# Optimization experiments

Measured on AMD Instinct MI355X. Metric: run time of the kernel, lower is better.

## Reference

```python
import jax, jax.numpy as jnp
import numpy as np

B, S, T, D, H, FF = 2, 512, 64, 256, 8, 1024
DK = D // H
EPS = 1e-5


def setup_inputs() -> dict:
    key = jax.random.key(0)
    ks = jax.random.split(key, 24)
    sc = 1.0 / np.sqrt(D)
    inp = {"x": jax.random.normal(ks[0], (B, S, T, D), jnp.float32)}
    names = ["tq", "tk", "tv", "to", "sq", "sk", "sv", "so"]
    for i, n in enumerate(names):
        inp[n + "_w"] = jax.random.normal(ks[1 + 2 * i], (D, D), jnp.float32) * sc
        inp[n + "_b"] = jax.random.normal(ks[2 + 2 * i], (D,), jnp.float32) * sc
    inp["fc1_w"] = jax.random.normal(ks[17], (D, FF), jnp.float32) * sc
    inp["fc1_b"] = jnp.zeros((FF,), jnp.float32)
    inp["fc2_w"] = jax.random.normal(ks[18], (FF, D), jnp.float32) * (1.0 / np.sqrt(FF))
    inp["fc2_b"] = jnp.zeros((D,), jnp.float32)
    inp["ln1_w"] = jnp.ones((D,), jnp.float32)
    inp["ln1_b"] = jnp.zeros((D,), jnp.float32)
    inp["ln2_w"] = jnp.ones((D,), jnp.float32)
    inp["ln2_b"] = jnp.zeros((D,), jnp.float32)
    return inp


def _heads(x, w, b):
    # (B,S,T,D) -> (B,H,S,T,DK)
    Bx, Sx, Tx, Dx = x.shape
    return (x @ w + b).reshape(Bx, Sx, Tx, H, Dx // H).transpose(0, 3, 1, 2, 4)


def _merge(o, w, b):
    # (B,H,S,T,DK) -> (B,S,T,D)
    Bx, Hx, Sx, Tx, dk = o.shape
    return o.transpose(0, 2, 3, 1, 4).reshape(Bx, Sx, Tx, Hx * dk) @ w + b


def _ln(x, g, b):
    m = jnp.mean(x, -1, keepdims=True)
    v = jnp.mean((x - m) ** 2, -1, keepdims=True)
    return (x - m) * jax.lax.rsqrt(v + EPS) * g + b


def _forward(x, tq_w, tq_b, tk_w, tk_b, tv_w, tv_b, to_w, to_b,
             sq_w, sq_b, sk_w, sk_b, sv_w, sv_b, so_w, so_b,
             fc1_w, fc1_b, fc2_w, fc2_b, ln1_w, ln1_b, ln2_w, ln2_b):
    scale = 1.0 / np.sqrt(DK)
    # --- time attention (over T, independent per space point s) ---
    q = _heads(x, tq_w, tq_b)
    k = _heads(x, tk_w, tk_b)
    v = _heads(x, tv_w, tv_b)
    p = jax.nn.softmax(jnp.einsum('bhstd,bhsud->bhstu', q, k) * scale, axis=-1)
    tt = _merge(jnp.einsum('bhstu,bhsud->bhstd', p, v), to_w, to_b)
    # --- space attention (over S, independent per time step t) ---
    q = _heads(tt, sq_w, sq_b)
    k = _heads(tt, sk_w, sk_b)
    v = _heads(tt, sv_w, sv_b)
    p = jax.nn.softmax(jnp.einsum('bhstd,bhutd->bhtsu', q, k) * scale, axis=-1)
    so = _merge(jnp.einsum('bhtsu,bhutd->bhstd', p, v), so_w, so_b)
    # --- residual + post-LN, then FFN + residual + post-LN ---
    h = _ln(x + so, ln1_w, ln1_b)
    ff = jax.nn.relu(h @ fc1_w + fc1_b) @ fc2_w + fc2_b
    return _ln(h + ff, ln2_w, ln2_b)


def reference(x, tq_w, tq_b, tk_w, tk_b, tv_w, tv_b, to_w, to_b,
              sq_w, sq_b, sk_w, sk_b, sv_w, sv_b, so_w, so_b,
              fc1_w, fc1_b, fc2_w, fc2_b, ln1_w, ln1_b, ln2_w, ln2_b):
    return _forward(x, tq_w, tq_b, tk_w, tk_b, tv_w, tv_b, to_w, to_b,
                    sq_w, sq_b, sk_w, sk_b, sv_w, sv_b, so_w, so_b,
                    fc1_w, fc1_b, fc2_w, fc2_b, ln1_w, ln1_b, ln2_w, ln2_b)
```

## Files before the change

kernel.cpp:

```cpp
#include <hip/hip_runtime.h>
#include <hip/hip_bf16.h>

#define BB   2
#define SS   512
#define TT_  64
#define DD   256
#define HH   8
#define DKK  32
#define FFF  1024
#define NTOK 65536
#define EPSV 1e-5f
#define SCALE 0.17677669529663687f
#define S2F   0.25503486f
#define KPS  40
#define KP   40
#define VH   136
#define VP6  80

typedef unsigned short u16;
typedef unsigned int   u32;
typedef __attribute__((ext_vector_type(8))) short bf16x8;
typedef __attribute__((ext_vector_type(4))) short bf16x4;
typedef __attribute__((ext_vector_type(4))) float f32x4;

#if __has_builtin(__builtin_amdgcn_exp2f)
#define EXP2(x) __builtin_amdgcn_exp2f(x)
#else
#define EXP2(x) exp2f(x)
#endif

__device__ __forceinline__ float bf2f(u32 u) {
    union { u32 i; float f; } c; c.i = u << 16; return c.f;
}
__device__ __forceinline__ u16 f2bf(float f) {
    __hip_bfloat16 h = __float2bfloat16(f);
    return *reinterpret_cast<u16*>(&h);
}
__device__ __forceinline__ u32 cvtpk2(float lo, float hi) {
    float2 f; f.x = lo; f.y = hi;
    __hip_bfloat162 h2 = __float22bfloat162_rn(f);
    union { __hip_bfloat162 h; u32 u; } c; c.h = h2;
    return c.u;
}
__device__ __forceinline__ void load8v(const float* p, float* v) {
    *(float4*)(v)     = *(const float4*)(p);
    *(float4*)(v + 4) = *(const float4*)(p + 4);
}
__device__ __forceinline__ void load8v(const u16* p, float* v) {
    uint4 raw = *(const uint4*)(p);
    v[0] = bf2f(raw.x & 0xffffu); v[1] = bf2f(raw.x >> 16);
    v[2] = bf2f(raw.y & 0xffffu); v[3] = bf2f(raw.y >> 16);
    v[4] = bf2f(raw.z & 0xffffu); v[5] = bf2f(raw.z >> 16);
    v[6] = bf2f(raw.w & 0xffffu); v[7] = bf2f(raw.w >> 16);
}
__device__ __forceinline__ void load4v(const float* p, float* v) {
    float4 t = *(const float4*)p; v[0] = t.x; v[1] = t.y; v[2] = t.z; v[3] = t.w;
}
__device__ __forceinline__ void load4v(const u16* p, float* v) {
    uint2 raw = *(const uint2*)p;
    v[0] = bf2f(raw.x & 0xffffu); v[1] = bf2f(raw.x >> 16);
    v[2] = bf2f(raw.y & 0xffffu); v[3] = bf2f(raw.y >> 16);
}
__device__ __forceinline__ uint4 pack8bf(const float* v) {
    uint4 r;
    r.x = cvtpk2(v[0], v[1]); r.y = cvtpk2(v[2], v[3]);
    r.z = cvtpk2(v[4], v[5]); r.w = cvtpk2(v[6], v[7]);
    return r;
}
__device__ __forceinline__ uint2 pack4bf(const float* v) {
    uint2 r;
    r.x = cvtpk2(v[0], v[1]); r.y = cvtpk2(v[2], v[3]);
    return r;
}
__device__ __forceinline__ bf16x4 packbf4(const float* v) {
    union { uint2 u; bf16x4 h; } c;
    c.u = pack4bf(v);
    return c.h;
}
__device__ __forceinline__ void store4o(float* p, const float* v) {
    float4 t; t.x = v[0]; t.y = v[1]; t.z = v[2]; t.w = v[3];
    *(float4*)p = t;
}
__device__ __forceinline__ void store4o(u16* p, const float* v) {
    *(uint2*)p = pack4bf(v);
}
__device__ __forceinline__ float rload(const float* p) { return *p; }
__device__ __forceinline__ float rload(const u16* p)  { return bf2f(*p); }
__device__ __forceinline__ void sstore(float* p, float v) { *p = v; }
__device__ __forceinline__ void sstore(u16* p, float v)   { *p = f2bf(v); }
__device__ __forceinline__ void gl16(const u16* gsrc, u16* ldst) {
    __builtin_amdgcn_global_load_lds(
        (const __attribute__((address_space(1))) void*)gsrc,
        (__attribute__((address_space(3))) void*)ldst, 16, 0, 0);
}

#if __has_builtin(__builtin_amdgcn_mfma_f32_16x16x16bf16_1k)
__device__ __forceinline__ f32x4 mfma16(bf16x4 a, bf16x4 b, f32x4 c) {
    return __builtin_amdgcn_mfma_f32_16x16x16bf16_1k(a, b, c, 0, 0, 0);
}
#else
__device__ __forceinline__ f32x4 mfma16(bf16x4 a, bf16x4 b, f32x4 c) {
    asm("v_mfma_f32_16x16x16_bf16 %0, %1, %2, %0" : "+v"(c) : "v"(a), "v"(b));
    return c;
}
#endif

#define BF16_ONE ((short)0x3F80)

__global__ __launch_bounds__(256)
void transpose_w(const float* __restrict__ W, u16* __restrict__ WT, int K, int M,
                 float scale)
{
    __shared__ float t[32][33];
    const int mb = blockIdx.x * 32;
    const int kb = blockIdx.y * 32;
    const int lx = threadIdx.x & 31;
    const int ly = threadIdx.x >> 5;
    #pragma unroll
    for (int i = ly; i < 32; i += 8) t[i][lx] = W[(size_t)(kb + i) * M + mb + lx];
    __syncthreads();
    #pragma unroll
    for (int i = ly; i < 32; i += 8) WT[(size_t)(mb + i) * K + kb + lx] = f2bf(t[lx][i] * scale);
}

__global__ __launch_bounds__(256)
void pack_bias3(const float* __restrict__ a, const float* __restrict__ b,
                const float* __restrict__ c, float* __restrict__ out, float s0)
{
    const int i = threadIdx.x;
    out[i] = a[i] * s0; out[256 + i] = b[i]; out[512 + i] = c[i];
}

__global__ __launch_bounds__(256)
void fuse_to_sqkv_w(const float* __restrict__ to_w,
                    const float* __restrict__ sq_w, const float* __restrict__ sk_w,
                    const float* __restrict__ sv_w, u16* __restrict__ wt_out)
{
    const int m = blockIdx.x;
    const int k = threadIdx.x;
    const float* Wsq = (m < 256) ? sq_w : (m < 512 ? sk_w : sv_w);
    const int mc = m & 255;
    float acc = 0.f;
    for (int j = 0; j < 256; j++)
        acc += to_w[k * 256 + j] * Wsq[j * 256 + mc];
    if (m < 256) acc *= S2F;
    wt_out[m * 256 + k] = f2bf(acc);
}
__global__ __launch_bounds__(256)
void fuse_to_sqkv_b(const float* __restrict__ to_b,
                    const float* __restrict__ sq_w, const float* __restrict__ sk_w,
                    const float* __restrict__ sv_w,
                    const float* __restrict__ sq_b, const float* __restrict__ sk_b,
                    const float* __restrict__ sv_b, float* __restrict__ b_out)
{
    const int m = blockIdx.x * 256 + threadIdx.x;
    const float* Wsq = (blockIdx.x == 0) ? sq_w : (blockIdx.x == 1 ? sk_w : sv_w);
    const float* bs  = (blockIdx.x == 0) ? sq_b : (blockIdx.x == 1 ? sk_b : sv_b);
    const int mc = m & 255;
    float acc = bs[mc];
    for (int j = 0; j < 256; j++) acc += to_b[j] * Wsq[j * 256 + mc];
    if (blockIdx.x == 0) acc *= S2F;
    b_out[m] = acc;
}

__global__ __launch_bounds__(256)
void cvt_bf16(const float* __restrict__ in, u16* __restrict__ out, int n8)
{
    for (int i = blockIdx.x * blockDim.x + threadIdx.x; i < n8; i += gridDim.x * blockDim.x) {
        float v[8];
        load8v(in + (size_t)i * 8, v);
        *(uint4*)(out + (size_t)i * 8) = pack8bf(v);
    }
}

__global__ __launch_bounds__(512)
void gemm_bt6(const u16* __restrict__ A, int lda,
              const u16* __restrict__ WT,
              const float* __restrict__ bias, u16* __restrict__ C,
              int K, int M, int relu)
{
    __shared__ u16 As0[256 * 32];
    __shared__ u16 As1[256 * 32];
    __shared__ u16 Bs0[128 * 32];
    __shared__ u16 Bs1[128 * 32];
    const int tid  = threadIdx.x;
    const int wid  = tid >> 6;
    const int lane = tid & 63;
    const int l16  = lane & 15;
    const int kg   = lane >> 4;

    const int nwg = gridDim.x * gridDim.y;
    int lin = blockIdx.y * gridDim.x + blockIdx.x;
    lin = (lin & 7) * (nwg >> 3) + (lin >> 3);
    const int row0 = (lin / gridDim.x) * 256;
    const int col0 = (lin % gridDim.x) * 128;

    const int srow = lane >> 2;
    const int gchunk = ((lane & 3) ^ ((srow >> 1) & 3)) * 8;
    const int rchunk = (kg ^ ((l16 >> 1) & 3)) * 8;

    const u16* Abase = A  + (size_t)(row0 + srow) * lda + gchunk;
    const u16* Bbase = WT + (size_t)(col0 + wid * 16 + srow) * K + gchunk;

    f32x4 acc[2][8];
    #pragma unroll
    for (int fr = 0; fr < 2; fr++)
        #pragma unroll
        for (int fc = 0; fc < 8; fc++)
            acc[fr][fc] = (f32x4){0.f, 0.f, 0.f, 0.f};

#define STAGE_T(ASB, BSB, k0)                                                   \
    do {                                                                        \
        _Pragma("unroll")                                                       \
        for (int q = 0; q < 2; q++) {                                           \
            const int rbase = wid * 32 + q * 16;                                \
            gl16(Abase + (size_t)rbase * lda + (k0), &ASB[rbase * 32]);         \
        }                                                                       \
        gl16(Bbase + (k0), &BSB[wid * 16 * 32]);                                \
    } while (0)

#define COMPUTE_T(ASB, BSB)                                                     \
    do {                                                                        \
        bf16x8 af[2], bfr[8];                                                   \
        _Pragma("unroll")                                                       \
        for (int fr = 0; fr < 2; fr++)                                          \
            af[fr] = *(const bf16x8*)(&ASB[(wid * 32 + fr * 16 + l16) * 32 + rchunk]); \
        _Pragma("unroll")                                                       \
        for (int fc = 0; fc < 8; fc++)                                          \
            bfr[fc] = *(const bf16x8*)(&BSB[(fc * 16 + l16) * 32 + rchunk]);    \
        _Pragma("unroll")                                                       \
        for (int fr = 0; fr < 2; fr++)                                          \
            _Pragma("unroll")                                                   \
            for (int fc = 0; fc < 8; fc++)                                      \
                acc[fr][fc] = __builtin_amdgcn_mfma_f32_16x16x32_bf16(af[fr], bfr[fc], acc[fr][fc], 0, 0, 0); \
    } while (0)

    STAGE_T(As0, Bs0, 0);
    __syncthreads();

    for (int k0 = 0; k0 < K; k0 += 64) {
        if (k0 + 32 < K) STAGE_T(As1, Bs1, k0 + 32);
        COMPUTE_T(As0, Bs0);
        __syncthreads();
        if (k0 + 64 < K) STAGE_T(As0, Bs0, k0 + 64);
        COMPUTE_T(As1, Bs1);
        __syncthreads();
    }
#undef STAGE_T
#undef COMPUTE_T

    #pragma unroll
    for (int fr = 0; fr < 2; fr++) {
        #pragma unroll
        for (int fc = 0; fc < 8; fc++) {
            const int col = col0 + fc * 16 + l16;
            const float bv = bias[col];
            const int row = row0 + wid * 32 + fr * 16 + kg * 4;
            #pragma unroll
            for (int j = 0; j < 4; j += 2) {
                float x0 = acc[fr][fc][j]     + bv;
                float x1 = acc[fr][fc][j + 1] + bv;
                if (relu) { x0 = fmaxf(x0, 0.f); x1 = fmaxf(x1, 0.f); }
                const u32 pk = cvtpk2(x0, x1);
                C[(size_t)(row + j)     * M + col] = (u16)pk;
                C[(size_t)(row + j + 1) * M + col] = (u16)(pk >> 16);
            }
        }
    }
}

__global__ __launch_bounds__(512)
void gemm_bt6h(const u16* __restrict__ A, int lda,
               const u16* __restrict__ WT,
               const float* __restrict__ bias, u16* __restrict__ C,
               int K, int M, int relu)
{
    __shared__ u16 As0[128 * 32];
    __shared__ u16 As1[128 * 32];
    __shared__ u16 Bs0[128 * 32];
    __shared__ u16 Bs1[128 * 32];
    const int tid  = threadIdx.x;
    const int wid  = tid >> 6;
    const int lane = tid & 63;
    const int l16  = lane & 15;
    const int kg   = lane >> 4;

    const int nwg = gridDim.x * gridDim.y;
    int lin = blockIdx.y * gridDim.x + blockIdx.x;
    lin = (lin & 7) * (nwg >> 3) + (lin >> 3);
    const int row0 = (lin / gridDim.x) * 128;
    const int col0 = (lin % gridDim.x) * 128;

    const int srow = lane >> 2;
    const int gchunk = ((lane & 3) ^ ((srow >> 1) & 3)) * 8;
    const int rchunk = (kg ^ ((l16 >> 1) & 3)) * 8;

    const u16* Abase = A  + (size_t)(row0 + wid * 16 + srow) * lda + gchunk;
    const u16* Bbase = WT + (size_t)(col0 + wid * 16 + srow) * K + gchunk;

    f32x4 acc[8];
    #pragma unroll
    for (int fc = 0; fc < 8; fc++)
        acc[fc] = (f32x4){0.f, 0.f, 0.f, 0.f};

#define STAGE_H(ASB, BSB, k0)                                                   \
    do {                                                                        \
        gl16(Abase + (k0), &ASB[wid * 16 * 32]);                                \
        gl16(Bbase + (k0), &BSB[wid * 16 * 32]);                                \
    } while (0)

#define COMPUTE_H(ASB, BSB)                                                     \
    do {                                                                        \
        bf16x8 af, bfr[8];                                                      \
        af = *(const bf16x8*)(&ASB[(wid * 16 + l16) * 32 + rchunk]);            \
        _Pragma("unroll")                                                       \
        for (int fc = 0; fc < 8; fc++)                                          \
            bfr[fc] = *(const bf16x8*)(&BSB[(fc * 16 + l16) * 32 + rchunk]);    \
        _Pragma("unroll")                                                       \
        for (int fc = 0; fc < 8; fc++)                                          \
            acc[fc] = __builtin_amdgcn_mfma_f32_16x16x32_bf16(af, bfr[fc], acc[fc], 0, 0, 0); \
    } while (0)

    STAGE_H(As0, Bs0, 0);
    __syncthreads();

    for (int k0 = 0; k0 < K; k0 += 64) {
        if (k0 + 32 < K) STAGE_H(As1, Bs1, k0 + 32);
        COMPUTE_H(As0, Bs0);
        __syncthreads();
        if (k0 + 64 < K) STAGE_H(As0, Bs0, k0 + 64);
        COMPUTE_H(As1, Bs1);
        __syncthreads();
    }
#undef STAGE_H
#undef COMPUTE_H

    #pragma unroll
    for (int fc = 0; fc < 8; fc++) {
        const int col = col0 + fc * 16 + l16;
        const float bv = bias[col];
        const int row = row0 + wid * 16 + kg * 4;
        #pragma unroll
        for (int j = 0; j < 4; j += 2) {
            float x0 = acc[fc][j]     + bv;
            float x1 = acc[fc][j + 1] + bv;
            if (relu) { x0 = fmaxf(x0, 0.f); x1 = fmaxf(x1, 0.f); }
            const u32 pk = cvtpk2(x0, x1);
            C[(size_t)(row + j)     * M + col] = (u16)pk;
            C[(size_t)(row + j + 1) * M + col] = (u16)(pk >> 16);
        }
    }
}

template<typename TR, typename TO>
__global__ __launch_bounds__(512)
void gemm_ln(const u16* __restrict__ A, int lda,
             const u16* __restrict__ WT,
             const float* __restrict__ bias,
             const TR* __restrict__ R,
             const float* __restrict__ gw, const float* __restrict__ bw,
             TO* __restrict__ out, int K)
{
    __shared__ u16 As0[128 * 32];
    __shared__ u16 As1[128 * 32];
    __shared__ u16 Bs0[256 * 32];
    __shared__ u16 Bs1[256 * 32];
    const int tid  = threadIdx.x;
    const int wid  = tid >> 6;
    const int lane = tid & 63;
    const int l16  = lane & 15;
    const int kg   = lane >> 4;

    const int nwg = gridDim.x;
    int lin = blockIdx.x;
    lin = (lin & 7) * (nwg >> 3) + (lin >> 3);
    const int row0 = lin * 128;

    const int srow = lane >> 2;
    const int gchunk = ((lane & 3) ^ ((srow >> 1) & 3)) * 8;
    const int rchunk = (kg ^ ((l16 >> 1) & 3)) * 8;

    const u16* Abase = A  + (size_t)(row0 + wid * 16 + srow) * lda + gchunk;
    const u16* Bbase = WT + (size_t)(wid * 32 + srow) * K + gchunk;

    f32x4 acc[16];
    #pragma unroll
    for (int fc = 0; fc < 16; fc++)
        acc[fc] = (f32x4){0.f, 0.f, 0.f, 0.f};

#define STAGE_L(ASB, BSB, k0)                                                   \
    do {                                                                        \
        gl16(Abase + (k0), &ASB[wid * 16 * 32]);                                \
        _Pragma("unroll")                                                       \
        for (int q = 0; q < 2; q++) {                                           \
            const int rbase = wid * 32 + q * 16;                                \
            gl16(Bbase + (size_t)(q * 16) * K + (k0), &BSB[rbase * 32]);        \
        }                                                                       \
    } while (0)

#define COMPUTE_L(ASB, BSB)                                                     \
    do {                                                                        \
        bf16x8 af, bfr[16];                                                     \
        af = *(const bf16x8*)(&ASB[(wid * 16 + l16) * 32 + rchunk]);            \
        _Pragma("unroll")                                                       \
        for (int fc = 0; fc < 16; fc++)                                         \
            bfr[fc] = *(const bf16x8*)(&BSB[(fc * 16 + l16) * 32 + rchunk]);    \
        _Pragma("unroll")                                                       \
        for (int fc = 0; fc < 16; fc++)                                         \
            acc[fc] = __builtin_amdgcn_mfma_f32_16x16x32_bf16(af, bfr[fc], acc[fc], 0, 0, 0); \
    } while (0)

    STAGE_L(As0, Bs0, 0);
    __syncthreads();

    for (int k0 = 0; k0 < K; k0 += 64) {
        if (k0 + 32 < K) STAGE_L(As1, Bs1, k0 + 32);
        COMPUTE_L(As0, Bs0);
        __syncthreads();
        if (k0 + 64 < K) STAGE_L(As0, Bs0, k0 + 64);
        COMPUTE_L(As1, Bs1);
        __syncthreads();
    }
#undef STAGE_L
#undef COMPUTE_L

    float bia[16], gwv[16], bwv[16];
    #pragma unroll
    for (int fc = 0; fc < 16; fc++) {
        const int d = fc * 16 + l16;
        bia[fc] = bias[d]; gwv[fc] = gw[d]; bwv[fc] = bw[d];
    }
    #pragma unroll
    for (int j = 0; j < 4; j++) {
        const int row = row0 + wid * 16 + kg * 4 + j;
        const size_t rb = (size_t)row * DD + l16;
        float v[16];
        float s1 = 0.f, s2 = 0.f;
        #pragma unroll
        for (int fc = 0; fc < 16; fc++) {
            const float xv = acc[fc][j] + bia[fc] + rload(R + rb + fc * 16);
            v[fc] = xv; s1 += xv; s2 += xv * xv;
        }
        #pragma unroll
        for (int o = 1; o < 16; o <<= 1) { s1 += __shfl_xor(s1, o); s2 += __shfl_xor(s2, o); }
        const float mean = s1 * (1.f / DD);
        const float var  = s2 * (1.f / DD) - mean * mean;
        const float rs   = rsqrtf(var + EPSV);
        #pragma unroll
        for (int fc = 0; fc < 16; fc++)
            sstore(out + rb + fc * 16, (v[fc] - mean) * rs * gwv[fc] + bwv[fc]);
    }
}

__global__ __launch_bounds__(256)
void time_attn12(const u16* __restrict__ F, int ld, u16* __restrict__ O)
{
    __shared__ u16 Ks2[2][64 * KP];
    __shared__ u16 Vt2[2][32 * VP6];
    const int bid = blockIdx.x;
    const int tid  = threadIdx.x;
    const int wid  = tid >> 6;
    const int lane = tid & 63;
    const int l16  = lane & 15;
    const int g    = lane >> 4;

    #pragma unroll
    for (int it = 0; it < 2; it++) {
        const int i = tid + it * 256;
        const int tu = i >> 8, rr = (i >> 2) & 63, p = i & 3;
        const int tau = bid * 2 + tu;
        const size_t ga = ((size_t)(tau >> 3) * 64 + rr) * ld + (tau & 7) * DKK + 256 + p * 8;
        *(uint4*)&Ks2[tu][rr * KP + p * 8] = *(const uint4*)(F + ga);
    }
    #pragma unroll
    for (int it = 0; it < 2; it++) {
        const int i = tid + it * 256;
        const int tu = i >> 8, p = (i >> 6) & 3, rr = i & 63;
        const int tau = bid * 2 + tu;
        const size_t ga = ((size_t)(tau >> 3) * 64 + rr) * ld + (tau & 7) * DKK + 512 + p * 8;
        uint4 vv = *(const uint4*)(F + ga);
        const u16* vp = (const u16*)&vv;
        #pragma unroll
        for (int j = 0; j < 8; j++) Vt2[tu][(p * 8 + j) * VP6 + rr] = vp[j];
    }
    __syncthreads();

    const int tu  = wid >> 1;
    const int tau = bid * 2 + tu;
    const int hc  = (tau & 7) * DKK;
    const size_t n0 = (size_t)(tau >> 3) * 64;
    const int q0  = (wid & 1) * 32;
    const f32x4 z4 = (f32x4){0.f, 0.f, 0.f, 0.f};
    const bf16x4 vone = (bf16x4){BF16_ONE, BF16_ONE, BF16_ONE, BF16_ONE};

    bf16x8 qf[2];
    #pragma unroll
    for (int f = 0; f < 2; f++)
        qf[f] = *(const bf16x8*)(F + (n0 + q0 + f * 16 + l16) * ld + hc + g * 8);

    f32x4 s[2][4];
    #pragma unroll
    for (int kt = 0; kt < 4; kt++) {
        bf16x8 kf = *(const bf16x8*)&Ks2[tu][(kt * 16 + l16) * KP + g * 8];
        s[0][kt] = __builtin_amdgcn_mfma_f32_16x16x32_bf16(kf, qf[0], z4, 0, 0, 0);
        s[1][kt] = __builtin_amdgcn_mfma_f32_16x16x32_bf16(kf, qf[1], z4, 0, 0, 0);
    }

    bf16x4 pp[2][4];
    #pragma unroll
    for (int f = 0; f < 2; f++) {
        #pragma unroll
        for (int kt = 0; kt < 4; kt++) {
            float pv[4];
            #pragma unroll
            for (int j = 0; j < 4; j++) pv[j] = EXP2(s[f][kt][j]);
            pp[f][kt] = packbf4(pv);
        }
    }

    f32x4 o[2][2];
    f32x4 lacc[2];
    #pragma unroll
    for (int f = 0; f < 2; f++) {
        lacc[f] = z4;
        #pragma unroll
        for (int hh = 0; hh < 2; hh++)
            o[f][hh] = z4;
    }
    #pragma unroll
    for (int kt = 0; kt < 4; kt++) {
        bf16x4 vf[2];
        #pragma unroll
        for (int hh = 0; hh < 2; hh++)
            vf[hh] = *(const bf16x4*)&Vt2[tu][(hh * 16 + l16) * VP6 + kt * 16 + g * 4];
        #pragma unroll
        for (int f = 0; f < 2; f++) {
            o[f][0] = mfma16(pp[f][kt], vf[0], o[f][0]);
            o[f][1] = mfma16(pp[f][kt], vf[1], o[f][1]);
            lacc[f] = mfma16(pp[f][kt], vone, lacc[f]);
        }
    }

    #pragma unroll
    for (int f = 0; f < 2; f++) {
        float iv[4];
        #pragma unroll
        for (int j = 0; j < 4; j++) iv[j] = 1.f / lacc[f][j];
        #pragma unroll
        for (int hh = 0; hh < 2; hh++) {
            const u32 p0 = cvtpk2(o[f][hh][0] * iv[0], o[f][hh][1] * iv[1]);
            const u32 p1 = cvtpk2(o[f][hh][2] * iv[2], o[f][hh][3] * iv[3]);
            const size_t ga0 = (n0 + q0 + f * 16 + g * 4) * DD + hc + hh * 16 + l16;
            O[ga0]          = (u16)p0;
            O[ga0 + DD]     = (u16)(p0 >> 16);
            O[ga0 + 2 * DD] = (u16)p1;
            O[ga0 + 3 * DD] = (u16)(p1 >> 16);
        }
    }
}

__global__ __launch_bounds__(512, 4)
void space_attn16(u16* __restrict__ F, int ld)
{
    __shared__ u16 Ks[2][128 * KPS];
    __shared__ u16 Vt[2][32 * VH];
    const int bid = blockIdx.x;
    const int t  = bid & (TT_ - 1);
    const int h  = (bid >> 6) & (HH - 1);
    const int b  = bid >> 9;
    const int hc = h * DKK;
    const int tid  = threadIdx.x;
    const int wid  = tid >> 6;
    const int lane = tid & 63;
    const int l16  = lane & 15;
    const int g    = lane >> 4;

    const int kr = tid >> 2, kp = tid & 3;
    const int vr = tid & 127, vp = tid >> 7;
    const size_t rowstr = (size_t)TT_ * ld;
    const size_t base0  = ((size_t)(b * SS) * TT_ + t) * ld + hc;

    const int q0 = wid * 64;
    bf16x8 qf[4];
    #pragma unroll
    for (int f = 0; f < 4; f++) {
        const int s = q0 + f * 16 + l16;
        qf[f] = *(const bf16x8*)(F + base0 + (size_t)s * rowstr + g * 8);
    }

    uint4 kreg = *(const uint4*)(F + base0 + 256 + (size_t)kr * rowstr + kp * 8);
    uint4 vreg = *(const uint4*)(F + base0 + 512 + (size_t)vr * rowstr + vp * 8);
    *(uint4*)&Ks[0][kr * KPS + kp * 8] = kreg;
    {
        const u16* vpp = (const u16*)&vreg;
        #pragma unroll
        for (int j = 0; j < 8; j++) Vt[0][(vp * 8 + j) * VH + vr] = vpp[j];
    }
    __syncthreads();

    f32x4 o[4][2];
    f32x4 lacc[4];
    const f32x4 z4 = (f32x4){0.f, 0.f, 0.f, 0.f};
    const bf16x4 vone = (bf16x4){BF16_ONE, BF16_ONE, BF16_ONE, BF16_ONE};
    #pragma unroll
    for (int f = 0; f < 4; f++) {
        lacc[f] = z4;
        #pragma unroll
        for (int hh = 0; hh < 2; hh++)
            o[f][hh] = z4;
    }

    for (int qtr = 0; qtr < 4; qtr++) {
        const int cur = qtr & 1;
        if (qtr < 3) {
            const int key = (qtr + 1) * 128;
            kreg = *(const uint4*)(F + base0 + 256 + (size_t)(key + kr) * rowstr + kp * 8);
            vreg = *(const uint4*)(F + base0 + 512 + (size_t)(key + vr) * rowstr + vp * 8);
        }

        for (int kc2 = 0; kc2 < 4; kc2++) {
            bf16x8 kfa = *(const bf16x8*)&Ks[cur][(kc2 * 32 +      l16) * KPS + g * 8];
            bf16x8 kfb = *(const bf16x8*)&Ks[cur][(kc2 * 32 + 16 + l16) * KPS + g * 8];

            bf16x4 pa[4], pb[4];
            #pragma unroll
            for (int f = 0; f < 4; f++) {
                f32x4 sa = __builtin_amdgcn_mfma_f32_16x16x32_bf16(kfa, qf[f], z4, 0, 0, 0);
                f32x4 sb = __builtin_amdgcn_mfma_f32_16x16x32_bf16(kfb, qf[f], z4, 0, 0, 0);
                float pva[4], pvb[4];
                #pragma unroll
                for (int j = 0; j < 4; j++) pva[j] = EXP2(sa[j]);
                #pragma unroll
                for (int j = 0; j < 4; j++) pvb[j] = EXP2(sb[j]);
                pa[f] = packbf4(pva);
                pb[f] = packbf4(pvb);
            }

            bf16x4 va[2][2];
            #pragma unroll
            for (int hh = 0; hh < 2; hh++)
                #pragma unroll
                for (int u = 0; u < 2; u++)
                    va[hh][u] = *(const bf16x4*)&Vt[cur][(hh * 16 + l16) * VH + kc2 * 32 + u * 16 + g * 4];

            __builtin_amdgcn_s_setprio(1);
            #pragma unroll
            for (int f = 0; f < 4; f++) {
                #pragma unroll
                for (int hh = 0; hh < 2; hh++) {
                    o[f][hh] = mfma16(pa[f], va[hh][0], o[f][hh]);
                    o[f][hh] = mfma16(pb[f], va[hh][1], o[f][hh]);
                }
                lacc[f] = mfma16(pa[f], vone, lacc[f]);
                lacc[f] = mfma16(pb[f], vone, lacc[f]);
            }
            __builtin_amdgcn_s_setprio(0);
        }

        if (qtr < 3) {
            __syncthreads();
            *(uint4*)&Ks[cur ^ 1][kr * KPS + kp * 8] = kreg;
            const u16* vpp = (const u16*)&vreg;
            #pragma unroll
            for (int j = 0; j < 8; j++) Vt[cur ^ 1][(vp * 8 + j) * VH + vr] = vpp[j];
            __syncthreads();
        }
    }

    #pragma unroll
    for (int f = 0; f < 4; f++) {
        float iv[4];
        #pragma unroll
        for (int j = 0; j < 4; j++) iv[j] = 1.f / lacc[f][j];
        const int s = q0 + f * 16 + g * 4;
        #pragma unroll
        for (int hh = 0; hh < 2; hh++) {
            const u32 p0 = cvtpk2(o[f][hh][0] * iv[0], o[f][hh][1] * iv[1]);
            const u32 p1 = cvtpk2(o[f][hh][2] * iv[2], o[f][hh][3] * iv[3]);
            const size_t ga0 = base0 + (size_t)s * rowstr + hh * 16 + l16;
            F[ga0]              = (u16)p0;
            F[ga0 + rowstr]     = (u16)(p0 >> 16);
            F[ga0 + 2 * rowstr] = (u16)p1;
            F[ga0 + 3 * rowstr] = (u16)(p1 >> 16);
        }
    }
}

template<typename T1, typename TO>
__global__ __launch_bounds__(256)
void add_ln(const T1* __restrict__ X1, const u16* __restrict__ X2,
            const float* __restrict__ gw, const float* __restrict__ bw,
            TO* __restrict__ out)
{
    const int row  = blockIdx.x * 4 + (threadIdx.x >> 6);
    const int lane = threadIdx.x & 63;
    const size_t base = (size_t)row * DD + lane * 4;
    float v[4], w2[4];
    load4v(X1 + base, v);
    load4v(X2 + base, w2);
    v[0] += w2[0]; v[1] += w2[1]; v[2] += w2[2]; v[3] += w2[3];
    float s1 = v[0] + v[1] + v[2] + v[3];
    float s2 = v[0]*v[0] + v[1]*v[1] + v[2]*v[2] + v[3]*v[3];
    #pragma unroll
    for (int o = 1; o < 64; o <<= 1) { s1 += __shfl_xor(s1, o); s2 += __shfl_xor(s2, o); }
    const float mean = s1 * (1.f / DD);
    const float var  = s2 * (1.f / DD) - mean * mean;
    const float rs   = rsqrtf(var + EPSV);
    float o4[4];
    #pragma unroll
    for (int i = 0; i < 4; i++) {
        const int d = lane * 4 + i;
        o4[i] = (v[i] - mean) * rs * gw[d] + bw[d];
    }
    store4o(out + base, o4);
}

extern "C" void kernel_launch(void* const* d_in, const int* in_sizes, int n_in,
                              void* d_out, int out_size, void* d_ws, size_t ws_size,
                              hipStream_t stream)
{
    (void)in_sizes; (void)n_in; (void)out_size;
    const float* x     = (const float*)d_in[0];
    const float* tq_w  = (const float*)d_in[1];
    const float* tq_b  = (const float*)d_in[2];
    const float* tk_w  = (const float*)d_in[3];
    const float* tk_b  = (const float*)d_in[4];
    const float* tv_w  = (const float*)d_in[5];
    const float* tv_b  = (const float*)d_in[6];
    const float* to_w  = (const float*)d_in[7];
    const float* to_b  = (const float*)d_in[8];
    const float* sq_w  = (const float*)d_in[9];
    const float* sq_b  = (const float*)d_in[10];
    const float* sk_w  = (const float*)d_in[11];
    const float* sk_b  = (const float*)d_in[12];
    const float* sv_w  = (const float*)d_in[13];
    const float* sv_b  = (const float*)d_in[14];
    const float* so_w  = (const float*)d_in[15];
    const float* so_b  = (const float*)d_in[16];
    const float* fc1_w = (const float*)d_in[17];
    const float* fc1_b = (const float*)d_in[18];
    const float* fc2_w = (const float*)d_in[19];
    const float* fc2_b = (const float*)d_in[20];
    const float* ln1_w = (const float*)d_in[21];
    const float* ln1_b = (const float*)d_in[22];
    const float* ln2_w = (const float*)d_in[23];
    const float* ln2_b = (const float*)d_in[24];

    const size_t SLOT = (size_t)NTOK * DD;
    u16*   F  = (u16*)d_ws;
    u16*   OA = (u16*)d_out;
    float* HD = (float*)d_out;

    const bool ffn1 = ws_size >= 6 * SLOT * sizeof(u16);
    u16*   WTb = ffn1 ? ((u16*)d_ws + 4 * SLOT)
                      : (u16*)((char*)d_out + (61u << 20));
    float* BIb = ffn1 ? (float*)((u16*)d_ws + 4 * SLOT + 983040)
                      : (float*)((char*)d_out + (63u << 20));

    u16* wt_tqkv  = WTb;
    u16* wt_fused = wt_tqkv + 3 * 65536;
    u16* wt_so    = wt_fused + 3 * 65536;
    u16* wt_fc1   = wt_so + 65536;
    u16* wt_fc2   = wt_fc1 + 262144;
    float* b_tqkv  = BIb;
    float* b_fused = BIb + 768;

    dim3 blk(256);
    dim3 blk5(512);
    dim3 gT(DD / 32, DD / 32);

    transpose_w<<<gT, blk, 0, stream>>>(tq_w, wt_tqkv,              DD, DD, S2F);
    transpose_w<<<gT, blk, 0, stream>>>(tk_w, wt_tqkv + 65536,      DD, DD, 1.0f);
    transpose_w<<<gT, blk, 0, stream>>>(tv_w, wt_tqkv + 2 * 65536,  DD, DD, 1.0f);
    transpose_w<<<gT, blk, 0, stream>>>(so_w, wt_so, DD, DD, 1.0f);
    transpose_w<<<dim3(FFF / 32, DD / 32), blk, 0, stream>>>(fc1_w, wt_fc1, DD, FFF, 1.0f);
    transpose_w<<<dim3(DD / 32, FFF / 32), blk, 0, stream>>>(fc2_w, wt_fc2, FFF, DD, 1.0f);
    pack_bias3<<<1, blk, 0, stream>>>(tq_b, tk_b, tv_b, b_tqkv, S2F);
    fuse_to_sqkv_w<<<768, blk, 0, stream>>>(to_w, sq_w, sk_w, sv_w, wt_fused);
    fuse_to_sqkv_b<<<3, blk, 0, stream>>>(to_b, sq_w, sk_w, sv_w, sq_b, sk_b, sv_b, b_fused);

    cvt_bf16<<<2048, blk, 0, stream>>>(x, OA, (int)(SLOT / 8));

    dim3 gqkv(768 / 128, NTOK / 256);

    gemm_bt6<<<gqkv, blk5, 0, stream>>>(OA, DD, wt_tqkv, b_tqkv, F, DD, 768, 0);
    time_attn12<<<BB * HH * SS / 2, blk, 0, stream>>>(F, 768, OA);

    gemm_bt6<<<gqkv, blk5, 0, stream>>>(OA, DD, wt_fused, b_fused, F, DD, 768, 0);
    space_attn16<<<BB * HH * TT_, blk5, 0, stream>>>(F, 768);

    if (ffn1) {
        u16* HB   = (u16*)d_ws + 5 * SLOT;
        u16* W1FF = (u16*)d_ws;
        gemm_ln<float, u16><<<NTOK / 128, blk5, 0, stream>>>(
            F, 768, wt_so, so_b, x, ln1_w, ln1_b, HB, DD);
        gemm_bt6<<<dim3(FFF / 128, NTOK / 256), blk5, 0, stream>>>(
            HB, DD, wt_fc1, fc1_b, W1FF, DD, FFF, 1);
        gemm_ln<u16, float><<<NTOK / 128, blk5, 0, stream>>>(
            W1FF, FFF, wt_fc2, fc2_b, HB, ln2_w, ln2_b, HD, FFF);
    } else {
        u16* W0 = (u16*)d_ws;
        u16* W1 = W0 + SLOT;
        u16* W2 = W1 + SLOT;
        dim3 gd(DD / 128, NTOK / 256);
        gemm_bt6<<<gd, blk5, 0, stream>>>(F, 768, wt_so, so_b, OA, DD, DD, 0);
        add_ln<float, u16><<<NTOK / 4, blk, 0, stream>>>(x, OA, ln1_w, ln1_b, W0);
        for (int c = 0; c < 4; c++) {
            const size_t off = (size_t)c * 16384 * DD;
            gemm_bt6<<<dim3(FFF / 128, 16384 / 256), blk5, 0, stream>>>(W0 + off, DD, wt_fc1, fc1_b, W1, DD, FFF, 1);
            gemm_bt6h<<<dim3(DD / 128, 16384 / 128), blk5, 0, stream>>>(W1, FFF, wt_fc2, fc2_b, W2, FFF, DD, 0);
            add_ln<u16, float><<<16384 / 4, blk, 0, stream>>>(W0 + off, W2, ln2_w, ln2_b, HD + off);
        }
    }
}
```

Measured before the change: 406.3 us.

## Use 256-row tiles in fc2 GEMM+LayerNorm kernel to reuse B fragments

Adds a gemm_ln2 variant where each wave computes two 16-row fragments (256 rows per block) and shares each loaded B fragment across two MFMAs, halving B LDS reads and B global staging per output row. The fc2+LN2 launch switches to this kernel with half the blocks. COMPUTE_L in the original kernel is also restructured to load B fragments inside the MFMA loop, which lowers register pressure. The new kernel needs more accumulators and 64KB of LDS, which may lower occupancy, and it launches fewer blocks.

```diff
diff --git a/kernel.cpp b/kernel.cpp
--- a/kernel.cpp
+++ b/kernel.cpp
@@ -400,14 +400,12 @@
 
 #define COMPUTE_L(ASB, BSB)                                                     \
     do {                                                                        \
-        bf16x8 af, bfr[16];                                                     \
-        af = *(const bf16x8*)(&ASB[(wid * 16 + l16) * 32 + rchunk]);            \
-        _Pragma("unroll")                                                       \
-        for (int fc = 0; fc < 16; fc++)                                         \
-            bfr[fc] = *(const bf16x8*)(&BSB[(fc * 16 + l16) * 32 + rchunk]);    \
-        _Pragma("unroll")                                                       \
-        for (int fc = 0; fc < 16; fc++)                                         \
-            acc[fc] = __builtin_amdgcn_mfma_f32_16x16x32_bf16(af, bfr[fc], acc[fc], 0, 0, 0); \
+        bf16x8 af = *(const bf16x8*)(&ASB[(wid * 16 + l16) * 32 + rchunk]);     \
+        _Pragma("unroll")                                                       \
+        for (int fc = 0; fc < 16; fc++) {                                       \
+            bf16x8 bfr = *(const bf16x8*)(&BSB[(fc * 16 + l16) * 32 + rchunk]); \
+            acc[fc] = __builtin_amdgcn_mfma_f32_16x16x32_bf16(af, bfr, acc[fc], 0, 0, 0); \
+        }                                                                       \
     } while (0)
 
     STAGE_L(As0, Bs0, 0);
@@ -449,6 +447,113 @@
         #pragma unroll
         for (int fc = 0; fc < 16; fc++)
             sstore(out + rb + fc * 16, (v[fc] - mean) * rs * gwv[fc] + bwv[fc]);
+    }
+}
+
+template<typename TR, typename TO>
+__global__ __launch_bounds__(512)
+void gemm_ln2(const u16* __restrict__ A, int lda,
+              const u16* __restrict__ WT,
+              const float* __restrict__ bias,
+              const TR* __restrict__ R,
+              const float* __restrict__ gw, const float* __restrict__ bw,
+              TO* __restrict__ out, int K)
+{
+    __shared__ u16 As0[256 * 32];
+    __shared__ u16 As1[256 * 32];
+    __shared__ u16 Bs0[256 * 32];
+    __shared__ u16 Bs1[256 * 32];
+    const int tid  = threadIdx.x;
+    const int wid  = tid >> 6;
+    const int lane = tid & 63;
+    const int l16  = lane & 15;
+    const int kg   = lane >> 4;
+
+    const int nwg = gridDim.x;
+    int lin = blockIdx.x;
+    lin = (lin & 7) * (nwg >> 3) + (lin >> 3);
+    const int row0 = lin * 256;
+
+    const int srow = lane >> 2;
+    const int gchunk = ((lane & 3) ^ ((srow >> 1) & 3)) * 8;
+    const int rchunk = (kg ^ ((l16 >> 1) & 3)) * 8;
+
+    const u16* Abase = A  + (size_t)(row0 + wid * 32 + srow) * lda + gchunk;
+    const u16* Bbase = WT + (size_t)(wid * 32 + srow) * K + gchunk;
+
+    f32x4 acc[2][16];
+    #pragma unroll
+    for (int fr = 0; fr < 2; fr++)
+        #pragma unroll
+        for (int fc = 0; fc < 16; fc++)
+            acc[fr][fc] = (f32x4){0.f, 0.f, 0.f, 0.f};
+
+#define STAGE_L2(ASB, BSB, k0)                                                  \
+    do {                                                                        \
+        _Pragma("unroll")                                                       \
+        for (int q = 0; q < 2; q++) {                                           \
+            const int rbase = wid * 32 + q * 16;                                \
+            gl16(Abase + (size_t)(q * 16) * lda + (k0), &ASB[rbase * 32]);      \
+            gl16(Bbase + (size_t)(q * 16) * K   + (k0), &BSB[rbase * 32]);      \
+        }                                                                       \
+    } while (0)
+
+#define COMPUTE_L2(ASB, BSB)                                                    \
+    do {                                                                        \
+        bf16x8 af[2];                                                           \
+        _Pragma("unroll")                                                       \
+        for (int fr = 0; fr < 2; fr++)                                          \
+            af[fr] = *(const bf16x8*)(&ASB[(wid * 32 + fr * 16 + l16) * 32 + rchunk]); \
+        _Pragma("unroll")                                                       \
+        for (int fc = 0; fc < 16; fc++) {                                       \
+            bf16x8 bfr = *(const bf16x8*)(&BSB[(fc * 16 + l16) * 32 + rchunk]); \
+            acc[0][fc] = __builtin_amdgcn_mfma_f32_16x16x32_bf16(af[0], bfr, acc[0][fc], 0, 0, 0); \
+            acc[1][fc] = __builtin_amdgcn_mfma_f32_16x16x32_bf16(af[1], bfr, acc[1][fc], 0, 0, 0); \
+        }                                                                       \
+    } while (0)
+
+    STAGE_L2(As0, Bs0, 0);
+    __syncthreads();
+
+    for (int k0 = 0; k0 < K; k0 += 64) {
+        if (k0 + 32 < K) STAGE_L2(As1, Bs1, k0 + 32);
+        COMPUTE_L2(As0, Bs0);
+        __syncthreads();
+        if (k0 + 64 < K) STAGE_L2(As0, Bs0, k0 + 64);
+        COMPUTE_L2(As1, Bs1);
+        __syncthreads();
+    }
+#undef STAGE_L2
+#undef COMPUTE_L2
+
+    float bia[16], gwv[16], bwv[16];
+    #pragma unroll
+    for (int fc = 0; fc < 16; fc++) {
+        const int d = fc * 16 + l16;
+        bia[fc] = bias[d]; gwv[fc] = gw[d]; bwv[fc] = bw[d];
+    }
+    #pragma unroll
+    for (int fr = 0; fr < 2; fr++) {
+        #pragma unroll
+        for (int j = 0; j < 4; j++) {
+            const int row = row0 + wid * 32 + fr * 16 + kg * 4 + j;
+            const size_t rb = (size_t)row * DD + l16;
+            float v[16];
+            float s1 = 0.f, s2 = 0.f;
+            #pragma unroll
+            for (int fc = 0; fc < 16; fc++) {
+                const float xv = acc[fr][fc][j] + bia[fc] + rload(R + rb + fc * 16);
+                v[fc] = xv; s1 += xv; s2 += xv * xv;
+            }
+            #pragma unroll
+            for (int o = 1; o < 16; o <<= 1) { s1 += __shfl_xor(s1, o); s2 += __shfl_xor(s2, o); }
+            const float mean = s1 * (1.f / DD);
+            const float var  = s2 * (1.f / DD) - mean * mean;
+            const float rs   = rsqrtf(var + EPSV);
+            #pragma unroll
+            for (int fc = 0; fc < 16; fc++)
+                sstore(out + rb + fc * 16, (v[fc] - mean) * rs * gwv[fc] + bwv[fc]);
+        }
     }
 }
 
@@ -796,7 +901,7 @@
             F, 768, wt_so, so_b, x, ln1_w, ln1_b, HB, DD);
         gemm_bt6<<<dim3(FFF / 128, NTOK / 256), blk5, 0, stream>>>(
             HB, DD, wt_fc1, fc1_b, W1FF, DD, FFF, 1);
-        gemm_ln<u16, float><<<NTOK / 128, blk5, 0, stream>>>(
+        gemm_ln2<u16, float><<<NTOK / 256, blk5, 0, stream>>>(
             W1FF, FFF, wt_fc2, fc2_b, HB, ln2_w, ln2_b, HD, FFF);
     } else {
         u16* W0 = (u16*)d_ws;
```

After: 403.9 us. Within noise of the previous version (-0.6%).

## Enlarge GEMM+LayerNorm tile to 256 rows with 64-deep K stages; batch weight transposes

Applied to the files above, without the earlier changes.

The fused GEMM+LayerNorm kernel now computes 256 rows per workgroup, with two 16-row fragments per wave sharing each B fragment load. Each pipeline stage covers 64 of K instead of 32, split across two LDS buffers per operand. The goal is to halve weight reloads from LDS and global memory per output row and to halve the number of barriers. In exchange, LDS use grows to 128KB per block and the accumulator registers double, which may lower occupancy, and the grid halves to 256 blocks. Separately, four square weight transposes are merged into one launch using blockIdx.z.

```diff
diff --git a/kernel.cpp b/kernel.cpp
--- a/kernel.cpp
+++ b/kernel.cpp
@@ -124,6 +124,28 @@
 }
 
 __global__ __launch_bounds__(256)
+void transpose_w4(const float* __restrict__ W0, const float* __restrict__ W1,
+                  const float* __restrict__ W2, const float* __restrict__ W3,
+                  u16* __restrict__ T0, u16* __restrict__ T1,
+                  u16* __restrict__ T2, u16* __restrict__ T3, float s0)
+{
+    __shared__ float t[32][33];
+    const int z = blockIdx.z;
+    const float* W = (z == 0) ? W0 : (z == 1) ? W1 : (z == 2) ? W2 : W3;
+    u16*       WT = (z == 0) ? T0 : (z == 1) ? T1 : (z == 2) ? T2 : T3;
+    const float scale = (z == 0) ? s0 : 1.0f;
+    const int mb = blockIdx.x * 32;
+    const int kb = blockIdx.y * 32;
+    const int lx = threadIdx.x & 31;
+    const int ly = threadIdx.x >> 5;
+    #pragma unroll
+    for (int i = ly; i < 32; i += 8) t[i][lx] = W[(size_t)(kb + i) * DD + mb + lx];
+    __syncthreads();
+    #pragma unroll
+    for (int i = ly; i < 32; i += 8) WT[(size_t)(mb + i) * DD + kb + lx] = f2bf(t[lx][i] * scale);
+}
+
+__global__ __launch_bounds__(256)
 void pack_bias3(const float* __restrict__ a, const float* __restrict__ b,
                 const float* __restrict__ c, float* __restrict__ out, float s0)
 {
@@ -354,17 +376,21 @@
 
 template<typename TR, typename TO>
 __global__ __launch_bounds__(512)
-void gemm_ln(const u16* __restrict__ A, int lda,
-             const u16* __restrict__ WT,
-             const float* __restrict__ bias,
-             const TR* __restrict__ R,
-             const float* __restrict__ gw, const float* __restrict__ bw,
-             TO* __restrict__ out, int K)
-{
-    __shared__ u16 As0[128 * 32];
-    __shared__ u16 As1[128 * 32];
-    __shared__ u16 Bs0[256 * 32];
-    __shared__ u16 Bs1[256 * 32];
+void gemm_ln2(const u16* __restrict__ A, int lda,
+              const u16* __restrict__ WT,
+              const float* __restrict__ bias,
+              const TR* __restrict__ R,
+              const float* __restrict__ gw, const float* __restrict__ bw,
+              TO* __restrict__ out, int K)
+{
+    __shared__ u16 As0a[256 * 32];
+    __shared__ u16 As0b[256 * 32];
+    __shared__ u16 As1a[256 * 32];
+    __shared__ u16 As1b[256 * 32];
+    __shared__ u16 Bs0a[256 * 32];
+    __shared__ u16 Bs0b[256 * 32];
+    __shared__ u16 Bs1a[256 * 32];
+    __shared__ u16 Bs1b[256 * 32];
     const int tid  = threadIdx.x;
     const int wid  = tid >> 6;
     const int lane = tid & 63;
@@ -374,55 +400,63 @@
     const int nwg = gridDim.x;
     int lin = blockIdx.x;
     lin = (lin & 7) * (nwg >> 3) + (lin >> 3);
-    const int row0 = lin * 128;
+    const int row0 = lin * 256;
 
     const int srow = lane >> 2;
     const int gchunk = ((lane & 3) ^ ((srow >> 1) & 3)) * 8;
     const int rchunk = (kg ^ ((l16 >> 1) & 3)) * 8;
 
-    const u16* Abase = A  + (size_t)(row0 + wid * 16 + srow) * lda + gchunk;
+    const u16* Abase = A  + (size_t)(row0 + wid * 32 + srow) * lda + gchunk;
     const u16* Bbase = WT + (size_t)(wid * 32 + srow) * K + gchunk;
 
-    f32x4 acc[16];
-    #pragma unroll
-    for (int fc = 0; fc < 16; fc++)
-        acc[fc] = (f32x4){0.f, 0.f, 0.f, 0.f};
-
-#define STAGE_L(ASB, BSB, k0)                                                   \
+    f32x4 acc[2][16];
+    #pragma unroll
+    for (int fr = 0; fr < 2; fr++)
+        #pragma unroll
+        for (int fc = 0; fc < 16; fc++)
+            acc[fr][fc] = (f32x4){0.f, 0.f, 0.f, 0.f};
+
+#define STAGE_L2(ASA, ASB2, BSA, BSB2, k0)                                      \
     do {                                                                        \
-        gl16(Abase + (k0), &ASB[wid * 16 * 32]);                                \
         _Pragma("unroll")                                                       \
         for (int q = 0; q < 2; q++) {                                           \
             const int rbase = wid * 32 + q * 16;                                \
-            gl16(Bbase + (size_t)(q * 16) * K + (k0), &BSB[rbase * 32]);        \
+            gl16(Abase + (size_t)(q * 16) * lda + (k0),      &ASA[rbase * 32]); \
+            gl16(Abase + (size_t)(q * 16) * lda + (k0) + 32, &ASB2[rbase * 32]);\
+            gl16(Bbase + (size_t)(q * 16) * K   + (k0),      &BSA[rbase * 32]); \
+            gl16(Bbase + (size_t)(q * 16) * K   + (k0) + 32, &BSB2[rbase * 32]);\
         }                                                                       \
     } while (0)
 
-#define COMPUTE_L(ASB, BSB)                                                     \
+#define COMPUTE_L2(ASB, BSB)                                                    \
     do {                                                                        \
-        bf16x8 af, bfr[16];                                                     \
-        af = *(const bf16x8*)(&ASB[(wid * 16 + l16) * 32 + rchunk]);            \
+        bf16x8 af[2];                                                           \
         _Pragma("unroll")                                                       \
-        for (int fc = 0; fc < 16; fc++)                                         \
-            bfr[fc] = *(const bf16x8*)(&BSB[(fc * 16 + l16) * 32 + rchunk]);    \
+        for (int fr = 0; fr < 2; fr++)                                          \
+            af[fr] = *(const bf16x8*)(&ASB[(wid * 32 + fr * 16 + l16) * 32 + rchunk]); \
         _Pragma("unroll")                                                       \
-        for (int fc = 0; fc < 16; fc++)                                         \
-            acc[fc] = __builtin_amdgcn_mfma_f32_16x16x32_bf16(af, bfr[fc], acc[fc], 0, 0, 0); \
+        for (int fc = 0; fc < 16; fc++) {                                       \
+            bf16x8 bfr = *(const bf16x8*)(&BSB[(fc * 16 + l16) * 32 + rchunk]); \
+            acc[0][fc] = __builtin_amdgcn_mfma_f32_16x16x32_bf16(af[0], bfr, acc[0][fc], 0, 0, 0); \
+            acc[1][fc] = __builtin_amdgcn_mfma_f32_16x16x32_bf16(af[1], bfr, acc[1][fc], 0, 0, 0); \
+        }                                                                       \
     } while (0)
 
-    STAGE_L(As0, Bs0, 0);
+    STAGE_L2(As0a, As0b, Bs0a, Bs0b, 0);
     __syncthreads();
 
-    for (int k0 = 0; k0 < K; k0 += 64) {
-        if (k0 + 32 < K) STAGE_L(As1, Bs1, k0 + 32);
-        COMPUTE_L(As0, Bs0);
+    for (int k0 = 0; k0 < K; k0 += 128) {
+        if (k0 + 64 < K) STAGE_L2(As1a, As1b, Bs1a, Bs1b, k0 + 64);
+        COMPUTE_L2(As0a, Bs0a);
+        COMPUTE_L2(As0b, Bs0b);
         __syncthreads();
-        if (k0 + 64 < K) STAGE_L(As0, Bs0, k0 + 64);
-        COMPUTE_L(As1, Bs1);
+        if (k0 + 128 < K) STAGE_L2(As0a, As0b, Bs0a, Bs0b, k0 + 128);
+        COMPUTE_L2(As1a, Bs1a);
+        COMPUTE_L2(As1b, Bs1b);
         __syncthreads();
     }
-#undef STAGE_L
-#undef COMPUTE_L
+#undef STAGE_L2
+#undef COMPUTE_L2
 
     float bia[16], gwv[16], bwv[16];
     #pragma unroll
@@ -431,24 +465,27 @@
         bia[fc] = bias[d]; gwv[fc] = gw[d]; bwv[fc] = bw[d];
     }
     #pragma unroll
-    for (int j = 0; j < 4; j++) {
-        const int row = row0 + wid * 16 + kg * 4 + j;
-        const size_t rb = (size_t)row * DD + l16;
-        float v[16];
-        float s1 = 0.f, s2 = 0.f;
-        #pragma unroll
-        for (int fc = 0; fc < 16; fc++) {
-            const float xv = acc[fc][j] + bia[fc] + rload(R + rb + fc * 16);
-            v[fc] = xv; s1 += xv; s2 += xv * xv;
-        }
-        #pragma unroll
-        for (int o = 1; o < 16; o <<= 1) { s1 += __shfl_xor(s1, o); s2 += __shfl_xor(s2, o); }
-        const float mean = s1 * (1.f / DD);
-        const float var  = s2 * (1.f / DD) - mean * mean;
-        const float rs   = rsqrtf(var + EPSV);
-        #pragma unroll
-        for (int fc = 0; fc < 16; fc++)
-            sstore(out + rb + fc * 16, (v[fc] - mean) * rs * gwv[fc] + bwv[fc]);
+    for (int fr = 0; fr < 2; fr++) {
+        #pragma unroll
+        for (int j = 0; j < 4; j++) {
+            const int row = row0 + wid * 32 + fr * 16 + kg * 4 + j;
+            const size_t rb = (size_t)row * DD + l16;
+            float v[16];
+            float s1 = 0.f, s2 = 0.f;
+            #pragma unroll
+            for (int fc = 0; fc < 16; fc++) {
+                const float xv = acc[fr][fc][j] + bia[fc] + rload(R + rb + fc * 16);
+                v[fc] = xv; s1 += xv; s2 += xv * xv;
+            }
+            #pragma unroll
+            for (int o = 1; o < 16; o <<= 1) { s1 += __shfl_xor(s1, o); s2 += __shfl_xor(s2, o); }
+            const float mean = s1 * (1.f / DD);
+            const float var  = s2 * (1.f / DD) - mean * mean;
+            const float rs   = rsqrtf(var + EPSV);
+            #pragma unroll
+            for (int fc = 0; fc < 16; fc++)
+                sstore(out + rb + fc * 16, (v[fc] - mean) * rs * gwv[fc] + bwv[fc]);
+        }
     }
 }
 
@@ -767,12 +804,10 @@
 
     dim3 blk(256);
     dim3 blk5(512);
-    dim3 gT(DD / 32, DD / 32);
-
-    transpose_w<<<gT, blk, 0, stream>>>(tq_w, wt_tqkv,              DD, DD, S2F);
-    transpose_w<<<gT, blk, 0, stream>>>(tk_w, wt_tqkv + 65536,      DD, DD, 1.0f);
-    transpose_w<<<gT, blk, 0, stream>>>(tv_w, wt_tqkv + 2 * 65536,  DD, DD, 1.0f);
-    transpose_w<<<gT, blk, 0, stream>>>(so_w, wt_so, DD, DD, 1.0f);
+
+    transpose_w4<<<dim3(DD / 32, DD / 32, 4), blk, 0, stream>>>(
+        tq_w, tk_w, tv_w, so_w,
+        wt_tqkv, wt_tqkv + 65536, wt_tqkv + 2 * 65536, wt_so, S2F);
     transpose_w<<<dim3(FFF / 32, DD / 32), blk, 0, stream>>>(fc1_w, wt_fc1, DD, FFF, 1.0f);
     transpose_w<<<dim3(DD / 32, FFF / 32), blk, 0, stream>>>(fc2_w, wt_fc2, FFF, DD, 1.0f);
     pack_bias3<<<1, blk, 0, stream>>>(tq_b, tk_b, tv_b, b_tqkv, S2F);
@@ -792,11 +827,11 @@
     if (ffn1) {
         u16* HB   = (u16*)d_ws + 5 * SLOT;
         u16* W1FF = (u16*)d_ws;
-        gemm_ln<float, u16><<<NTOK / 128, blk5, 0, stream>>>(
+        gemm_ln2<float, u16><<<NTOK / 256, blk5, 0, stream>>>(
             F, 768, wt_so, so_b, x, ln1_w, ln1_b, HB, DD);
         gemm_bt6<<<dim3(FFF / 128, NTOK / 256), blk5, 0, stream>>>(
             HB, DD, wt_fc1, fc1_b, W1FF, DD, FFF, 1);
-        gemm_ln<u16, float><<<NTOK / 128, blk5, 0, stream>>>(
+        gemm_ln2<u16, float><<<NTOK / 256, blk5, 0, stream>>>(
             W1FF, FFF, wt_fc2, fc2_b, HB, ln2_w, ln2_b, HD, FFF);
     } else {
         u16* W0 = (u16*)d_ws;
```

Result: faster. 384.9 us, median of 3 (-5.3%).
